# Optimization experiments

Measured on AMD Instinct MI355X. Metric: run time of the kernel, lower is better.

## Reference

```python
import jax, jax.numpy as jnp
import numpy as np

VOCAB = 50257
EMB = 256
HID = 256
FORGET_BIAS = 1.0


def setup_inputs() -> dict:
    key = jax.random.key(0)
    ks = jax.random.split(key, 8)
    B, T = 16, 256
    s = 0.05
    return {
        "tokens": jax.random.randint(ks[0], (B, T), 0, VOCAB, dtype=jnp.int32),
        # embedding matrix init mimics tf.random_uniform(-1, 1)
        "emb": jax.random.uniform(ks[1], (VOCAB, EMB), jnp.float32, -1.0, 1.0),
        "W1": jax.random.normal(ks[2], (EMB + HID, 4 * HID), jnp.float32) * s,
        "b1": jnp.zeros((4 * HID,), jnp.float32),
        "W2": jax.random.normal(ks[3], (HID + HID, 4 * HID), jnp.float32) * s,
        "b2": jnp.zeros((4 * HID,), jnp.float32),
        "Wout": jax.random.normal(ks[4], (HID, VOCAB), jnp.float32) * s,
        "bout": jnp.zeros((VOCAB,), jnp.float32),
    }


def _lstm_cell(c, h, x, W, b):
    # BasicLSTMCell: gates = [x, h] @ W + b, split i, j, f, o
    g = jnp.concatenate([x, h], axis=-1) @ W + b
    i, j, f, o = jnp.split(g, 4, axis=-1)
    c_new = c * jax.nn.sigmoid(f + FORGET_BIAS) + jax.nn.sigmoid(i) * jnp.tanh(j)
    h_new = jnp.tanh(c_new) * jax.nn.sigmoid(o)
    return c_new, h_new


def reference(tokens, emb, W1, b1, W2, b2, Wout, bout):
    B, T = tokens.shape
    x = emb[tokens]                 # [B, T, EMB] embedding lookup
    x_tm = jnp.swapaxes(x, 0, 1)    # [T, B, EMB] time-major for scan

    def step(carry, xt):
        c1, h1, c2, h2 = carry
        c1, h1 = _lstm_cell(c1, h1, xt, W1, b1)
        c2, h2 = _lstm_cell(c2, h2, h1, W2, b2)
        return (c1, h1, c2, h2), h2

    z = jnp.zeros((B, HID), x.dtype)
    _, hs = jax.lax.scan(step, (z, z, z, z), x_tm)  # hs: [T, B, HID]
    hs = jnp.swapaxes(hs, 0, 1).reshape(-1, HID)    # [B*T, HID] (batch-major flatten as in tf.reshape)
    logits = hs @ Wout + bout                        # [B*T, VOCAB]
    return logits
```

## Files before the change

### kernel.cpp

```cpp
#include <hip/hip_runtime.h>
#include <hip/hip_bf16.h>
#include <stdint.h>

#define BB 16
#define TT 256
#define HH 256
#define EE 256
#define GG 1024
#define VV 50257
#define NN 4096

typedef unsigned short u16;
typedef __attribute__((ext_vector_type(8))) short short8;
typedef __attribute__((ext_vector_type(4))) float f32x4;

__device__ __forceinline__ float sigm(float x){
    float e = __builtin_amdgcn_exp2f(fminf(-x*1.44269504f, 60.0f));
    return 1.0f/(1.0f+e);
}
__device__ __forceinline__ float tanha(float x){
    float e = __builtin_amdgcn_exp2f(fminf(x*2.885390082f, 60.0f));
    return (e-1.0f)/(e+1.0f);
}
__device__ __forceinline__ u16 f2bf(float f){
    uint32_t u = __float_as_uint(f);
    u = (u + 0x7FFFu + ((u>>16)&1u)) >> 16;
    return (u16)u;
}
__device__ __forceinline__ void st32_coh(uint32_t* p, uint32_t v){
    __hip_atomic_store(p, v, __ATOMIC_RELAXED, __HIP_MEMORY_SCOPE_AGENT);
}
__device__ __forceinline__ uint32_t poll_pair(const uint32_t* p){
    uint32_t v = __hip_atomic_load(p, __ATOMIC_RELAXED, __HIP_MEMORY_SCOPE_AGENT);
    while ((v & 0xFFFFu) == 0xFFFFu || (v >> 16) == 0xFFFFu){
        __builtin_amdgcn_s_sleep(1);
        v = __hip_atomic_load(p, __ATOMIC_RELAXED, __HIP_MEMORY_SCOPE_AGENT);
    }
    return v;
}
__device__ __forceinline__ void gl_lds16(const void* g, void* s){
    __builtin_amdgcn_global_load_lds((const __attribute__((address_space(1))) unsigned int*)g,
                                     (__attribute__((address_space(3))) unsigned int*)s, 16, 0, 0);
}

__global__ __launch_bounds__(256) void g1_kernel(const int* __restrict__ tok, const float* __restrict__ emb,
                                                 const float* __restrict__ W1, const float* __restrict__ b1,
                                                 float* __restrict__ G1t){
    __shared__ float xs[64*64];
    __shared__ float wsm[64*64];
    int n0 = blockIdx.x * 64;
    int g0 = blockIdx.y * 64;
    int tid = threadIdx.x;
    int sl = tid & 63;
    int kk = (tid >> 6) * 16;
    int mytok = tok[n0 + sl];
    float acc[4][4] = {};
    int ni = tid & 15, gi = tid >> 4;
    for (int kc = 0; kc < 4; ++kc){
        int k0 = kc*64;
        __syncthreads();
        #pragma unroll
        for (int i4 = 0; i4 < 4; ++i4){
            float4 xv = *(const float4*)(&emb[(size_t)mytok*EE + k0 + kk + i4*4]);
            xs[(kk+i4*4+0)*64 + sl] = xv.x;
            xs[(kk+i4*4+1)*64 + sl] = xv.y;
            xs[(kk+i4*4+2)*64 + sl] = xv.z;
            xs[(kk+i4*4+3)*64 + sl] = xv.w;
        }
        #pragma unroll
        for (int i = 0; i < 16; ++i){
            wsm[(kk+i)*64 + sl] = W1[(size_t)(k0+kk+i)*GG + g0 + sl];
        }
        __syncthreads();
        for (int k = 0; k < 64; ++k){
            float4 av = *(const float4*)(&xs[k*64 + ni*4]);
            float4 bv = *(const float4*)(&wsm[k*64 + gi*4]);
            float a_[4] = {av.x, av.y, av.z, av.w};
            float b_[4] = {bv.x, bv.y, bv.z, bv.w};
            #pragma unroll
            for (int i = 0; i < 4; ++i)
                #pragma unroll
                for (int j = 0; j < 4; ++j)
                    acc[i][j] += a_[i]*b_[j];
        }
    }
    #pragma unroll
    for (int i = 0; i < 4; ++i){
        int n = n0 + ni*4 + i;
        int b = n >> 8;
        int tt_ = n & 255;
        float4 o;
        o.x = acc[i][0] + b1[g0+gi*4+0];
        o.y = acc[i][1] + b1[g0+gi*4+1];
        o.z = acc[i][2] + b1[g0+gi*4+2];
        o.w = acc[i][3] + b1[g0+gi*4+3];
        *(float4*)(&G1t[(size_t)(tt_*16 + b)*GG + g0 + gi*4]) = o;
    }
}

__global__ __launch_bounds__(1024) void persist_kernel(
        const float* __restrict__ G1t, const float* __restrict__ W1,
        const float* __restrict__ W2, const float* __restrict__ b2,
        const float* __restrict__ Wout, u16* __restrict__ WoutT,
        u16* __restrict__ h1y, u16* __restrict__ h2b){
    __shared__ __align__(16) char smem[12288];
    const int bid = blockIdx.x;
    const int tid = threadIdx.x;

    if (bid >= 96){
        u16* tile = (u16*)smem;
        const int r = tid >> 4, i = tid & 15;
        for (int tau = bid - 96; tau < 786*4; tau += 128){
            int ky = tau / 786;
            int nx = tau - ky*786;
            int n0 = nx*64, k0 = ky*64;
            #pragma unroll
            for (int jj = 0; jj < 4; ++jj){
                int n = n0 + i*4 + jj;
                float f = (n < VV) ? Wout[(size_t)(k0 + r)*VV + n] : 0.0f;
                tile[(i*4 + jj)*66 + r] = f2bf(f);
            }
            __syncthreads();
            {
                int kl = i*4;
                uint2 v;
                v.x = (uint32_t)tile[r*66 + kl+0] | ((uint32_t)tile[r*66 + kl+1] << 16);
                v.y = (uint32_t)tile[r*66 + kl+2] | ((uint32_t)tile[r*66 + kl+3] << 16);
                *(uint2*)(&WoutT[(size_t)(n0 + r)*256 + k0 + kl]) = v;
            }
            __syncthreads();
        }
        return;
    }

    const int g  = bid & 7;
    const int rr = bid >> 3;
    const int l  = tid & 63;
    const int wv = tid >> 6;
    uint32_t* h1y32 = (uint32_t*)h1y;
    uint32_t* h2b32 = (uint32_t*)h2b;

    if (rr < 4){
        const int r1 = rr;
        const int gate = wv >> 2, usub = wv & 3;
        const int colw = gate*HH + 64*r1 + 16*usub;
        short8 wf[8];
        {
            const int col = colw + (l & 15);
            const int kb = (l >> 4) << 3;
            #pragma unroll
            for (int kk = 0; kk < 8; ++kk){
                short8 s;
                #pragma unroll
                for (int j = 0; j < 8; ++j)
                    s[j] = (short)f2bf(W1[(size_t)(HH + kk*32 + kb + j)*GG + col]);
                wf[kk] = s;
            }
        }
        u16*      hA   = (u16*)smem;
        uint32_t* hA32 = (uint32_t*)smem;
        float*    gm   = (float*)(smem + 1024);
        const int ab = tid >> 5, ap_ = tid & 31;
        float creg0 = 0.f, creg1 = 0.f;

        for (int t = 0; t < TT; ++t){
            float c0 = 0.f, c1 = 0.f;
            if (l < 16){
                c0 = G1t[((size_t)t*BB + 2*g + 0)*GG + colw + l];
                c1 = G1t[((size_t)t*BB + 2*g + 1)*GG + colw + l];
            }
            f32x4 acc = {c0, c1, 0.f, 0.f};
            if (t > 0){
                if (tid < 256){
                    int b = tid >> 7, p = tid & 127;
                    hA32[b*128 + p] = poll_pair(&h1y32[(((size_t)(t-1)*8 + g)*2 + b)*128 + p]);
                }
                __syncthreads();
                const u16* app = hA + (l & 1)*256 + ((l >> 4) << 3);
                f32x4 acc2 = {0.f, 0.f, 0.f, 0.f};
                #pragma unroll
                for (int kk = 0; kk < 4; ++kk){
                    acc  = __builtin_amdgcn_mfma_f32_16x16x32_bf16(*(const short8*)(app + (2*kk  )*32), wf[2*kk  ], acc , 0, 0, 0);
                    acc2 = __builtin_amdgcn_mfma_f32_16x16x32_bf16(*(const short8*)(app + (2*kk+1)*32), wf[2*kk+1], acc2, 0, 0, 0);
                }
                acc[0] += acc2[0];
                acc[1] += acc2[1];
            }
            if (l < 16){
                gm[(gate*64 + usub*16 + l)*2 + 0] = acc[0];
                gm[(gate*64 + usub*16 + l)*2 + 1] = acc[1];
            }
            __syncthreads();
            if (tid < 64){
                int u0 = 2*ap_, u1 = 2*ap_ + 1;
                float gi0 = gm[(0*64 + u0)*2 + ab], gi1 = gm[(0*64 + u1)*2 + ab];
                float gj0 = gm[(1*64 + u0)*2 + ab], gj1 = gm[(1*64 + u1)*2 + ab];
                float gf0 = gm[(2*64 + u0)*2 + ab], gf1 = gm[(2*64 + u1)*2 + ab];
                float go0 = gm[(3*64 + u0)*2 + ab], go1 = gm[(3*64 + u1)*2 + ab];
                float cn0 = creg0 * sigm(gf0 + 1.0f) + sigm(gi0)*tanha(gj0);
                float cn1 = creg1 * sigm(gf1 + 1.0f) + sigm(gi1)*tanha(gj1);
                float hn0 = tanha(cn0)*sigm(go0);
                float hn1 = tanha(cn1)*sigm(go1);
                creg0 = cn0; creg1 = cn1;
                uint32_t pk = (uint32_t)f2bf(hn0) | ((uint32_t)f2bf(hn1) << 16);
                st32_coh(&h1y32[(((size_t)t*8 + g)*2 + ab)*128 + 32*r1 + ap_], pk);
            }
            __syncthreads();
        }
    } else {
        const int r2 = rr - 4;
        const int nt = wv >> 1, kh = wv & 1;
        const int gate = nt >> 1, usub = nt & 1;
        const int colw = gate*HH + 32*r2 + 16*usub;
        short8 wf[8];
        {
            const int col = colw + (l & 15);
            const int kb = (l >> 4) << 3;
            #pragma unroll
            for (int kk = 0; kk < 8; ++kk){
                short8 s;
                #pragma unroll
                for (int j = 0; j < 8; ++j)
                    s[j] = (short)f2bf(W2[(size_t)(kh*256 + kk*32 + kb + j)*GG + col]);
                wf[kk] = s;
            }
        }
        u16*      uB   = (u16*)smem;
        uint32_t* uB32 = (uint32_t*)smem;
        float*    gm   = (float*)(smem + 2048);
        const int ab = tid >> 4, ap_ = tid & 15;
        float creg0 = 0.f, creg1 = 0.f;
        float bvs[4][2];
        if (tid < 32){
            #pragma unroll
            for (int gg = 0; gg < 4; ++gg){
                bvs[gg][0] = b2[gg*HH + 32*r2 + 2*ap_];
                bvs[gg][1] = b2[gg*HH + 32*r2 + 2*ap_ + 1];
            }
        }

        for (int tt = 0; tt < TT; ++tt){
            if (tid < 512){
                int b = tid >> 8, q = tid & 255;
                uint32_t v;
                if (q < 128)
                    v = poll_pair(&h1y32[(((size_t)tt*8 + g)*2 + b)*128 + q]);
                else if (tt > 0)
                    v = poll_pair(&h2b32[((size_t)(2*g + b)*TT + (tt-1))*128 + (q - 128)]);
                else
                    v = 0;
                uB32[b*256 + q] = v;
            }
            __syncthreads();
            f32x4 acc = {0.f, 0.f, 0.f, 0.f};
            f32x4 acc2 = {0.f, 0.f, 0.f, 0.f};
            const u16* app = uB + (l & 1)*512 + kh*256 + ((l >> 4) << 3);
            #pragma unroll
            for (int kk = 0; kk < 4; ++kk){
                acc  = __builtin_amdgcn_mfma_f32_16x16x32_bf16(*(const short8*)(app + (2*kk  )*32), wf[2*kk  ], acc , 0, 0, 0);
                acc2 = __builtin_amdgcn_mfma_f32_16x16x32_bf16(*(const short8*)(app + (2*kk+1)*32), wf[2*kk+1], acc2, 0, 0, 0);
            }
            acc[0] += acc2[0];
            acc[1] += acc2[1];
            if (l < 16){
                gm[((gate*32 + usub*16 + l)*2 + 0)*2 + kh] = acc[0];
                gm[((gate*32 + usub*16 + l)*2 + 1)*2 + kh] = acc[1];
            }
            __syncthreads();
            if (tid < 32){
                int u0 = 2*ap_, u1 = 2*ap_ + 1;
                float gi0 = gm[((0*32 + u0)*2 + ab)*2 + 0] + gm[((0*32 + u0)*2 + ab)*2 + 1] + bvs[0][0];
                float gi1 = gm[((0*32 + u1)*2 + ab)*2 + 0] + gm[((0*32 + u1)*2 + ab)*2 + 1] + bvs[0][1];
                float gj0 = gm[((1*32 + u0)*2 + ab)*2 + 0] + gm[((1*32 + u0)*2 + ab)*2 + 1] + bvs[1][0];
                float gj1 = gm[((1*32 + u1)*2 + ab)*2 + 0] + gm[((1*32 + u1)*2 + ab)*2 + 1] + bvs[1][1];
                float gf0 = gm[((2*32 + u0)*2 + ab)*2 + 0] + gm[((2*32 + u0)*2 + ab)*2 + 1] + bvs[2][0];
                float gf1 = gm[((2*32 + u1)*2 + ab)*2 + 0] + gm[((2*32 + u1)*2 + ab)*2 + 1] + bvs[2][1];
                float go0 = gm[((3*32 + u0)*2 + ab)*2 + 0] + gm[((3*32 + u0)*2 + ab)*2 + 1] + bvs[3][0];
                float go1 = gm[((3*32 + u1)*2 + ab)*2 + 0] + gm[((3*32 + u1)*2 + ab)*2 + 1] + bvs[3][1];
                float cn0 = creg0 * sigm(gf0 + 1.0f) + sigm(gi0)*tanha(gj0);
                float cn1 = creg1 * sigm(gf1 + 1.0f) + sigm(gi1)*tanha(gj1);
                float hn0 = tanha(cn0)*sigm(go0);
                float hn1 = tanha(cn1)*sigm(go1);
                creg0 = cn0; creg1 = cn1;
                uint32_t pk = (uint32_t)f2bf(hn0) | ((uint32_t)f2bf(hn1) << 16);
                st32_coh(&h2b32[((size_t)(2*g + ab)*TT + tt)*128 + 16*r2 + ap_], pk);
            }
            __syncthreads();
        }
    }
}

__global__ __launch_bounds__(256, 4) void out_gemm(const u16* __restrict__ A, const u16* __restrict__ Bt,
                                                   const float* __restrict__ bout, float* __restrict__ out){
    __shared__ __align__(16) char smem[36864];
    u16* ldsA = (u16*)smem;
    u16* ldsB = (u16*)(smem + 16384);
    float* ldsF = (float*)smem;
    const int bid = blockIdx.x;
    const int x   = bid & 7;
    const int wgl = bid >> 3;
    const int mb  = x*4 + (wgl & 3);
    const int nb  = wgl >> 2;
    const int m0 = mb*128, n0 = nb*128;
    const int tid = threadIdx.x;
    const int l = tid & 63;
    const int wv = tid >> 6;
    const int wm = wv >> 1, wn = wv & 1;
    const int lr = l & 15, lh = l >> 4;

    f32x4 acc[4][4];
    #pragma unroll
    for (int mf = 0; mf < 4; ++mf)
        #pragma unroll
        for (int nf = 0; nf < 4; ++nf) acc[mf][nf] = (f32x4){0.f,0.f,0.f,0.f};

    #pragma unroll
    for (int ks = 0; ks < 4; ++ks){
        #pragma unroll
        for (int j = 0; j < 4; ++j){
            int f = j*256 + tid;
            int row = f >> 3;
            int kps = (f & 7) ^ (row & 7);
            gl_lds16(A  + (size_t)(m0+row)*256 + ks*64 + kps*8, (char*)ldsA + f*16);
            gl_lds16(Bt + (size_t)(n0+row)*256 + ks*64 + kps*8, (char*)ldsB + f*16);
        }
        __syncthreads();
        #pragma unroll
        for (int ksub = 0; ksub < 2; ++ksub){
            short8 af[4], bf[4];
            const int kp = ksub*4 + lh;
            #pragma unroll
            for (int mf = 0; mf < 4; ++mf){
                int row = wm*64 + mf*16 + lr;
                af[mf] = *(const short8*)((const char*)ldsA + row*128 + ((kp ^ (row&7)) << 4));
            }
            #pragma unroll
            for (int nf = 0; nf < 4; ++nf){
                int row = wn*64 + nf*16 + lr;
                bf[nf] = *(const short8*)((const char*)ldsB + row*128 + ((kp ^ (row&7)) << 4));
            }
            #pragma unroll
            for (int mf = 0; mf < 4; ++mf)
                #pragma unroll
                for (int nf = 0; nf < 4; ++nf)
                    acc[mf][nf] = __builtin_amdgcn_mfma_f32_16x16x32_bf16(af[mf], bf[nf], acc[mf][nf], 0, 0, 0);
        }
        __syncthreads();
    }

    for (int h = 0; h < 2; ++h){
        if (wm == h){
            #pragma unroll
            for (int nf = 0; nf < 4; ++nf){
                int col = wn*64 + nf*16 + lr;
                int gcol = n0 + col;
                float bb2 = (gcol < VV) ? bout[gcol] : 0.0f;
                #pragma unroll
                for (int mf = 0; mf < 4; ++mf)
                    #pragma unroll
                    for (int r = 0; r < 4; ++r)
                        ldsF[(mf*16 + lh*4 + r)*132 + col] = acc[mf][nf][r] + bb2;
            }
        }
        __syncthreads();
        #pragma unroll
        for (int j = 0; j < 8; ++j){
            int f = j*256 + tid;
            int row = f >> 5;
            int c4 = (f & 31)*4;
            int gcol = n0 + c4;
            f32x4 v = *(const f32x4*)(ldsF + row*132 + c4);
            int grow = m0 + h*64 + row;
            if (gcol + 3 < VV){
                *(f32x4*)(&out[(size_t)grow*VV + gcol]) = v;
            } else {
                #pragma unroll
                for (int e = 0; e < 4; ++e)
                    if (gcol + e < VV) out[(size_t)grow*VV + gcol + e] = v[e];
            }
        }
        __syncthreads();
    }
}

extern "C" void kernel_launch(void* const* d_in, const int* in_sizes, int n_in,
                              void* d_out, int out_size, void* d_ws, size_t ws_size,
                              hipStream_t stream) {
    const int*   tok  = (const int*)d_in[0];
    const float* emb  = (const float*)d_in[1];
    const float* W1   = (const float*)d_in[2];
    const float* b1   = (const float*)d_in[3];
    const float* W2   = (const float*)d_in[4];
    const float* b2   = (const float*)d_in[5];
    const float* Wout = (const float*)d_in[6];
    const float* bout = (const float*)d_in[7];
    float* out = (float*)d_out;
    char* ws = (char*)d_ws;

    u16*   h1y   = (u16*)  (ws);
    u16*   h2b   = (u16*)  (ws + 2097152);
    float* G1t   = (float*)(ws + 4194304);
    u16*   WoutT = (u16*)  (ws + 4194304 + 16777216);

    hipMemsetAsync(ws, 0xFF, 4194304, stream);
    g1_kernel<<<dim3(64, 16), 256, 0, stream>>>(tok, emb, W1, b1, G1t);
    persist_kernel<<<224, 1024, 0, stream>>>(G1t, W1, W2, b2, Wout, WoutT, h1y, h2b);
    out_gemm<<<12576, 256, 0, stream>>>(h2b, WoutT, bout, out);
}
```

Measured before the change: 773.7 us.

## Interleave gate columns per wave to compute LSTM cell via shuffles, drop LDS barrier

Rearranges each wave's MFMA output columns so the four gates (i,j,f,o) of a hidden unit sit in adjacent lanes. The cell update is then computed in-register with wave shuffles instead of going through LDS and an extra __syncthreads per step. Layer 2 now uses 4 groups of 64 units with full-K (16 MFMA) per wave instead of splitting K across waves. As a result, fewer blocks run the recurrence and more blocks transpose Wout. The aim is to shorten the serial per-timestep critical path, at the cost of more registers per lane and more MFMAs per wave in layer 2.

```diff
diff --git a/kernel.cpp b/kernel.cpp
--- a/kernel.cpp
+++ b/kernel.cpp
@@ -107,10 +107,10 @@
     const int bid = blockIdx.x;
     const int tid = threadIdx.x;
 
-    if (bid >= 96){
+    if (bid >= 64){
         u16* tile = (u16*)smem;
         const int r = tid >> 4, i = tid & 15;
-        for (int tau = bid - 96; tau < 786*4; tau += 128){
+        for (int tau = bid - 64; tau < 786*4; tau += 160){
             int ky = tau / 786;
             int nx = tau - ky*786;
             int n0 = nx*64, k0 = ky*64;
@@ -137,107 +137,83 @@
     const int rr = bid >> 3;
     const int l  = tid & 63;
     const int wv = tid >> 6;
+    const int c  = l & 15;
+    const int kb = (l >> 4) << 3;
+    const int b4 = l & 12;
     uint32_t* h1y32 = (uint32_t*)h1y;
     uint32_t* h2b32 = (uint32_t*)h2b;
 
     if (rr < 4){
         const int r1 = rr;
-        const int gate = wv >> 2, usub = wv & 3;
-        const int colw = gate*HH + 64*r1 + 16*usub;
+        const int colg = (c&3)*HH + 64*r1 + 4*wv + (c>>2);
         short8 wf[8];
-        {
-            const int col = colw + (l & 15);
-            const int kb = (l >> 4) << 3;
-            #pragma unroll
-            for (int kk = 0; kk < 8; ++kk){
-                short8 s;
-                #pragma unroll
-                for (int j = 0; j < 8; ++j)
-                    s[j] = (short)f2bf(W1[(size_t)(HH + kk*32 + kb + j)*GG + col]);
-                wf[kk] = s;
-            }
+        #pragma unroll
+        for (int kk = 0; kk < 8; ++kk){
+            short8 s;
+            #pragma unroll
+            for (int j = 0; j < 8; ++j)
+                s[j] = (short)f2bf(W1[(size_t)(HH + kk*32 + kb + j)*GG + colg]);
+            wf[kk] = s;
         }
         u16*      hA   = (u16*)smem;
         uint32_t* hA32 = (uint32_t*)smem;
-        float*    gm   = (float*)(smem + 1024);
-        const int ab = tid >> 5, ap_ = tid & 31;
         float creg0 = 0.f, creg1 = 0.f;
 
         for (int t = 0; t < TT; ++t){
             float c0 = 0.f, c1 = 0.f;
             if (l < 16){
-                c0 = G1t[((size_t)t*BB + 2*g + 0)*GG + colw + l];
-                c1 = G1t[((size_t)t*BB + 2*g + 1)*GG + colw + l];
+                c0 = G1t[((size_t)t*BB + 2*g + 0)*GG + colg];
+                c1 = G1t[((size_t)t*BB + 2*g + 1)*GG + colg];
             }
             f32x4 acc = {c0, c1, 0.f, 0.f};
+            f32x4 acc2 = {0.f, 0.f, 0.f, 0.f};
             if (t > 0){
                 if (tid < 256){
                     int b = tid >> 7, p = tid & 127;
                     hA32[b*128 + p] = poll_pair(&h1y32[(((size_t)(t-1)*8 + g)*2 + b)*128 + p]);
                 }
                 __syncthreads();
-                const u16* app = hA + (l & 1)*256 + ((l >> 4) << 3);
-                f32x4 acc2 = {0.f, 0.f, 0.f, 0.f};
+                const u16* app = hA + (l & 1)*256 + kb;
                 #pragma unroll
                 for (int kk = 0; kk < 4; ++kk){
                     acc  = __builtin_amdgcn_mfma_f32_16x16x32_bf16(*(const short8*)(app + (2*kk  )*32), wf[2*kk  ], acc , 0, 0, 0);
                     acc2 = __builtin_amdgcn_mfma_f32_16x16x32_bf16(*(const short8*)(app + (2*kk+1)*32), wf[2*kk+1], acc2, 0, 0, 0);
                 }
-                acc[0] += acc2[0];
-                acc[1] += acc2[1];
-            }
-            if (l < 16){
-                gm[(gate*64 + usub*16 + l)*2 + 0] = acc[0];
-                gm[(gate*64 + usub*16 + l)*2 + 1] = acc[1];
-            }
-            __syncthreads();
-            if (tid < 64){
-                int u0 = 2*ap_, u1 = 2*ap_ + 1;
-                float gi0 = gm[(0*64 + u0)*2 + ab], gi1 = gm[(0*64 + u1)*2 + ab];
-                float gj0 = gm[(1*64 + u0)*2 + ab], gj1 = gm[(1*64 + u1)*2 + ab];
-                float gf0 = gm[(2*64 + u0)*2 + ab], gf1 = gm[(2*64 + u1)*2 + ab];
-                float go0 = gm[(3*64 + u0)*2 + ab], go1 = gm[(3*64 + u1)*2 + ab];
-                float cn0 = creg0 * sigm(gf0 + 1.0f) + sigm(gi0)*tanha(gj0);
-                float cn1 = creg1 * sigm(gf1 + 1.0f) + sigm(gi1)*tanha(gj1);
-                float hn0 = tanha(cn0)*sigm(go0);
-                float hn1 = tanha(cn1)*sigm(go1);
-                creg0 = cn0; creg1 = cn1;
-                uint32_t pk = (uint32_t)f2bf(hn0) | ((uint32_t)f2bf(hn1) << 16);
-                st32_coh(&h1y32[(((size_t)t*8 + g)*2 + ab)*128 + 32*r1 + ap_], pk);
+            }
+            float v0 = acc[0] + acc2[0], v1 = acc[1] + acc2[1];
+            float gi0=__shfl(v0,b4+0), gj0=__shfl(v0,b4+1), gf0=__shfl(v0,b4+2), go0=__shfl(v0,b4+3);
+            float gi1=__shfl(v1,b4+0), gj1=__shfl(v1,b4+1), gf1=__shfl(v1,b4+2), go1=__shfl(v1,b4+3);
+            float cn0 = creg0*sigm(gf0+1.f) + sigm(gi0)*tanha(gj0);
+            float cn1 = creg1*sigm(gf1+1.f) + sigm(gi1)*tanha(gj1);
+            float hn0 = tanha(cn0)*sigm(go0);
+            float hn1 = tanha(cn1)*sigm(go1);
+            creg0 = cn0; creg1 = cn1;
+            uint32_t p0 = f2bf(hn0), p1 = f2bf(hn1);
+            uint32_t q0 = (uint32_t)__shfl((int)p0, (l+4)&63);
+            uint32_t q1 = (uint32_t)__shfl((int)p1, (l+4)&63);
+            if (l == 0 || l == 8){
+                uint32_t pi = 32*r1 + 2*wv + (l>>3);
+                st32_coh(&h1y32[(((size_t)t*8 + g)*2 + 0)*128 + pi], p0 | (q0<<16));
+                st32_coh(&h1y32[(((size_t)t*8 + g)*2 + 1)*128 + pi], p1 | (q1<<16));
             }
             __syncthreads();
         }
     } else {
         const int r2 = rr - 4;
-        const int nt = wv >> 1, kh = wv & 1;
-        const int gate = nt >> 1, usub = nt & 1;
-        const int colw = gate*HH + 32*r2 + 16*usub;
-        short8 wf[8];
-        {
-            const int col = colw + (l & 15);
-            const int kb = (l >> 4) << 3;
-            #pragma unroll
-            for (int kk = 0; kk < 8; ++kk){
-                short8 s;
-                #pragma unroll
-                for (int j = 0; j < 8; ++j)
-                    s[j] = (short)f2bf(W2[(size_t)(kh*256 + kk*32 + kb + j)*GG + col]);
-                wf[kk] = s;
-            }
-        }
+        const int colg = (c&3)*HH + 64*r2 + 4*wv + (c>>2);
+        short8 wf[16];
+        #pragma unroll
+        for (int kk = 0; kk < 16; ++kk){
+            short8 s;
+            #pragma unroll
+            for (int j = 0; j < 8; ++j)
+                s[j] = (short)f2bf(W2[(size_t)(kk*32 + kb + j)*GG + colg]);
+            wf[kk] = s;
+        }
+        float bvg = b2[colg];
         u16*      uB   = (u16*)smem;
         uint32_t* uB32 = (uint32_t*)smem;
-        float*    gm   = (float*)(smem + 2048);
-        const int ab = tid >> 4, ap_ = tid & 15;
         float creg0 = 0.f, creg1 = 0.f;
-        float bvs[4][2];
-        if (tid < 32){
-            #pragma unroll
-            for (int gg = 0; gg < 4; ++gg){
-                bvs[gg][0] = b2[gg*HH + 32*r2 + 2*ap_];
-                bvs[gg][1] = b2[gg*HH + 32*r2 + 2*ap_ + 1];
-            }
-        }
 
         for (int tt = 0; tt < TT; ++tt){
             if (tid < 512){
@@ -252,38 +228,29 @@
                 uB32[b*256 + q] = v;
             }
             __syncthreads();
-            f32x4 acc = {0.f, 0.f, 0.f, 0.f};
+            f32x4 acc  = {0.f, 0.f, 0.f, 0.f};
             f32x4 acc2 = {0.f, 0.f, 0.f, 0.f};
-            const u16* app = uB + (l & 1)*512 + kh*256 + ((l >> 4) << 3);
-            #pragma unroll
-            for (int kk = 0; kk < 4; ++kk){
+            const u16* app = uB + (l & 1)*512 + kb;
+            #pragma unroll
+            for (int kk = 0; kk < 8; ++kk){
                 acc  = __builtin_amdgcn_mfma_f32_16x16x32_bf16(*(const short8*)(app + (2*kk  )*32), wf[2*kk  ], acc , 0, 0, 0);
                 acc2 = __builtin_amdgcn_mfma_f32_16x16x32_bf16(*(const short8*)(app + (2*kk+1)*32), wf[2*kk+1], acc2, 0, 0, 0);
             }
-            acc[0] += acc2[0];
-            acc[1] += acc2[1];
-            if (l < 16){
-                gm[((gate*32 + usub*16 + l)*2 + 0)*2 + kh] = acc[0];
-                gm[((gate*32 + usub*16 + l)*2 + 1)*2 + kh] = acc[1];
-            }
-            __syncthreads();
-            if (tid < 32){
-                int u0 = 2*ap_, u1 = 2*ap_ + 1;
-                float gi0 = gm[((0*32 + u0)*2 + ab)*2 + 0] + gm[((0*32 + u0)*2 + ab)*2 + 1] + bvs[0][0];
-                float gi1 = gm[((0*32 + u1)*2 + ab)*2 + 0] + gm[((0*32 + u1)*2 + ab)*2 + 1] + bvs[0][1];
-                float gj0 = gm[((1*32 + u0)*2 + ab)*2 + 0] + gm[((1*32 + u0)*2 + ab)*2 + 1] + bvs[1][0];
-                float gj1 = gm[((1*32 + u1)*2 + ab)*2 + 0] + gm[((1*32 + u1)*2 + ab)*2 + 1] + bvs[1][1];
-                float gf0 = gm[((2*32 + u0)*2 + ab)*2 + 0] + gm[((2*32 + u0)*2 + ab)*2 + 1] + bvs[2][0];
-                float gf1 = gm[((2*32 + u1)*2 + ab)*2 + 0] + gm[((2*32 + u1)*2 + ab)*2 + 1] + bvs[2][1];
-                float go0 = gm[((3*32 + u0)*2 + ab)*2 + 0] + gm[((3*32 + u0)*2 + ab)*2 + 1] + bvs[3][0];
-                float go1 = gm[((3*32 + u1)*2 + ab)*2 + 0] + gm[((3*32 + u1)*2 + ab)*2 + 1] + bvs[3][1];
-                float cn0 = creg0 * sigm(gf0 + 1.0f) + sigm(gi0)*tanha(gj0);
-                float cn1 = creg1 * sigm(gf1 + 1.0f) + sigm(gi1)*tanha(gj1);
-                float hn0 = tanha(cn0)*sigm(go0);
-                float hn1 = tanha(cn1)*sigm(go1);
-                creg0 = cn0; creg1 = cn1;
-                uint32_t pk = (uint32_t)f2bf(hn0) | ((uint32_t)f2bf(hn1) << 16);
-                st32_coh(&h2b32[((size_t)(2*g + ab)*TT + tt)*128 + 16*r2 + ap_], pk);
+            float v0 = acc[0] + acc2[0] + bvg, v1 = acc[1] + acc2[1] + bvg;
+            float gi0=__shfl(v0,b4+0), gj0=__shfl(v0,b4+1), gf0=__shfl(v0,b4+2), go0=__shfl(v0,b4+3);
+            float gi1=__shfl(v1,b4+0), gj1=__shfl(v1,b4+1), gf1=__shfl(v1,b4+2), go1=__shfl(v1,b4+3);
+            float cn0 = creg0*sigm(gf0+1.f) + sigm(gi0)*tanha(gj0);
+            float cn1 = creg1*sigm(gf1+1.f) + sigm(gi1)*tanha(gj1);
+            float hn0 = tanha(cn0)*sigm(go0);
+            float hn1 = tanha(cn1)*sigm(go1);
+            creg0 = cn0; creg1 = cn1;
+            uint32_t p0 = f2bf(hn0), p1 = f2bf(hn1);
+            uint32_t q0 = (uint32_t)__shfl((int)p0, (l+4)&63);
+            uint32_t q1 = (uint32_t)__shfl((int)p1, (l+4)&63);
+            if (l == 0 || l == 8){
+                uint32_t pi = 32*r2 + 2*wv + (l>>3);
+                st32_coh(&h2b32[((size_t)(2*g + 0)*TT + tt)*128 + pi], p0 | (q0<<16));
+                st32_coh(&h2b32[((size_t)(2*g + 1)*TT + tt)*128 + pi], p1 | (q1<<16));
             }
             __syncthreads();
         }
```

After: 1.082 ms. 1.4x slower.
